# Optimization experiments

Hardware: AMD Instinct MI355X
Metric: run time of the kernel (lower is better)

Reference implementation:

```python
import jax, jax.numpy as jnp
import numpy as np

B, L, D, H = 2, 2048, 2048, 16
Dh = D // H
THETA = 500000.0


def _init_rope(dim, seq_len, n_heads):
    # Returns freqs_cis of shape (1, seq_len, 1, head_dim//2, 2) -> [..., 0]=cos, [..., 1]=sin
    hd = dim // n_heads
    inv_freqs = 1.0 / (THETA ** (jnp.arange(0, hd, 2, dtype=jnp.float32) / hd))
    t = jnp.arange(seq_len, dtype=jnp.float32)
    freqs = jnp.outer(t, inv_freqs).astype(jnp.float32)  # (L, hd/2)
    fc = jnp.stack([jnp.cos(freqs)[None, :, None, :],
                    jnp.sin(freqs)[None, :, None, :]], axis=3)  # (1, L, 1, 2, hd/2)
    return fc.transpose(0, 1, 2, 4, 3)  # (1, L, 1, hd/2, 2)


def _apply_rope(q, k, freqs_cis):
    def rotate(x):
        x2 = x.reshape(*x.shape[:-1], -1, 2)  # (B, L, H, Dh/2, 2)
        f = freqs_cis[:, :x.shape[1]]
        cos, sin = f[..., 0], f[..., 1]
        r = jnp.stack([x2[..., 0] * cos - x2[..., 1] * sin,
                       x2[..., 1] * cos + x2[..., 0] * sin], axis=-1)
        return r.reshape(*x.shape)
    return rotate(q), rotate(k)


def setup_inputs() -> dict:
    key = jax.random.key(0)
    kx, kq, kk, kv, ko = jax.random.split(key, 5)
    scale = 1.0 / np.sqrt(D)
    x = jax.random.normal(kx, (B, L, D), dtype=jnp.float32)
    Wq = jax.random.normal(kq, (D, H, Dh), dtype=jnp.float32) * scale
    Wk = jax.random.normal(kk, (D, H, Dh), dtype=jnp.float32) * scale
    Wv = jax.random.normal(kv, (D, H, Dh), dtype=jnp.float32) * scale
    Wo = jax.random.normal(ko, (D, D), dtype=jnp.float32) * scale
    return {"x": x, "Wq": Wq, "Wk": Wk, "Wv": Wv, "Wo": Wo}


def reference(x, Wq, Wk, Wv, Wo):
    freqs_cis = _init_rope(D, L, H)
    q = jnp.einsum('bld,dhk->blhk', x, Wq)  # (B, L, H, Dh)
    k = jnp.einsum('bld,dhk->blhk', x, Wk)
    v = jnp.einsum('bld,dhk->blhk', x, Wv)
    q, k = _apply_rope(q, k, freqs_cis)
    q = q / (Dh ** 0.5)
    att = jnp.einsum('bqhd,bkhd->bhqk', q, k)  # (B, H, L, L)
    Lq = x.shape[1]
    mask = jnp.tril(jnp.ones((1, 1, Lq, Lq), dtype=jnp.bool_))
    neg_inf = jnp.finfo(jnp.float32).min
    att = jnp.where(mask, att, neg_inf)
    att = jax.nn.softmax(att, axis=-1)
    out = jnp.einsum('bhqk,bkhd->bqhd', att, v)  # (B, L, H, Dh)
    out = out.reshape(x.shape)
    return jnp.einsum('bld,de->ble', out, Wo)
```

## Files before the change

### kernel.cpp

```cpp
#include <hip/hip_runtime.h>

typedef unsigned short u16;
typedef unsigned int u32;

#define Bb 2
#define Lc 2048
#define Dc 2048
#define Hc 16
#define DhC 128

typedef __bf16 bf16x8 __attribute__((ext_vector_type(8)));
typedef float f32x4 __attribute__((ext_vector_type(4)));
typedef float f32x16 __attribute__((ext_vector_type(16)));

__device__ __forceinline__ u16 f2b(float f) {
  u32 u = __float_as_uint(f);
  u32 r = (u + 0x7fffu + ((u >> 16) & 1u)) >> 16;
  return (u16)r;
}
__device__ __forceinline__ float b2f(u16 u) {
  return __uint_as_float(((u32)u) << 16);
}

__device__ __forceinline__ u32 cvtpk(float lo, float hi) {
  u32 r;
  asm("v_cvt_pk_bf16_f32 %0, %1, %2" : "=v"(r) : "v"(lo), "v"(hi));
  return r;
}

__device__ __forceinline__ void gll16(const void* g, void* l) {
  __builtin_amdgcn_global_load_lds(
      (const __attribute__((address_space(1))) u32*)g,
      (__attribute__((address_space(3))) u32*)l, 16, 0, 0);
}

__global__ __launch_bounds__(256) void sniff_dtype(const u16* __restrict__ x,
                                                   int* __restrict__ flag) {
  __shared__ int bad;
  if (threadIdx.x == 0) bad = 0;
  __syncthreads();
  int local = 0;
  for (int i = threadIdx.x; i < 65536; i += 256) {
    float v = fabsf(b2f(x[i]));
    if (!(v < 1000.f)) local = 1;
  }
  if (local) atomicOr(&bad, 1);
  __syncthreads();
  if (threadIdx.x == 0) *flag = bad;
}

__global__ __launch_bounds__(256) void conv_x(const void* __restrict__ in,
                                              u16* __restrict__ out,
                                              const int* __restrict__ flag) {
  const int f32 = *flag;
  const int i0 = (blockIdx.x * 256 + threadIdx.x) * 4;
  if (f32) {
    const float* p = (const float*)in;
#pragma unroll
    for (int j = 0; j < 4; j++) out[i0 + j] = f2b(p[i0 + j]);
  } else {
    const u16* p = (const u16*)in;
#pragma unroll
    for (int j = 0; j < 4; j++) out[i0 + j] = p[i0 + j];
  }
}

__global__ __launch_bounds__(256) void transpose2d_conv(const void* __restrict__ in,
                                                        u16* __restrict__ out,
                                                        const int* __restrict__ flag) {
  __shared__ __align__(16) u16 tile[64][65];
  const int f32 = *flag;
  const int r0 = blockIdx.y * 64, c0 = blockIdx.x * 64;
  const int tc = threadIdx.x & 63, tr4 = threadIdx.x >> 6;
#pragma unroll
  for (int p = 0; p < 16; p++) {
    int r = tr4 + p * 4;
    size_t idx = (size_t)(r0 + r) * 2048 + c0 + tc;
    tile[r][tc] = f32 ? f2b(((const float*)in)[idx]) : ((const u16*)in)[idx];
  }
  __syncthreads();
#pragma unroll
  for (int p = 0; p < 16; p++) {
    int rr = tr4 + p * 4;
    out[(size_t)(c0 + rr) * 2048 + r0 + tc] = tile[tc][rr];
  }
}

template <typename OutT>
__device__ __forceinline__ void gemm_bt_core(const u16* __restrict__ A,
                                             const u16* __restrict__ Bt,
                                             OutT* __restrict__ C) {
  constexpr int K = 2048, N = 2048;
  __shared__ __align__(16) u16 As[128 * 64];
  __shared__ __align__(16) u16 Bs[128 * 64];
  const int tid = threadIdx.x;
  const int lane = tid & 63, wid = tid >> 6;
  const int wm = (wid >> 1) * 64, wn = (wid & 1) * 64;
  const int m0 = blockIdx.x * 128, n0 = blockIdx.y * 128;
  const int quad = lane >> 4, l15 = lane & 15;
  const int sw = l15 & 7;

  const f32x4 fz = {0.f, 0.f, 0.f, 0.f};
  f32x4 acc[4][4];
#pragma unroll
  for (int i = 0; i < 4; i++)
#pragma unroll
    for (int j = 0; j < 4; j++) acc[i][j] = fz;

  const int srl = (lane >> 3);
  const int ssl = lane & 7;

  for (int k0 = 0; k0 < K; k0 += 64) {
#pragma unroll
    for (int p = 0; p < 4; p++) {
      const int r = p * 32 + wid * 8 + srl;
      const int c = ssl ^ (r & 7);
      u16* lb = As + (p * 256 + wid * 64) * 8;
      gll16(A + (size_t)(m0 + r) * K + k0 + c * 8, lb);
    }
#pragma unroll
    for (int p = 0; p < 4; p++) {
      const int r = p * 32 + wid * 8 + srl;
      const int c = ssl ^ (r & 7);
      u16* lb = Bs + (p * 256 + wid * 64) * 8;
      gll16(Bt + (size_t)(n0 + r) * K + k0 + c * 8, lb);
    }
    __syncthreads();
#pragma unroll
    for (int ks = 0; ks < 2; ks++) {
      bf16x8 af[4], bfr[4];
#pragma unroll
      for (int t = 0; t < 4; t++) {
        const int cc = ((ks * 4 + quad) ^ sw) * 8;
        af[t]  = *(const bf16x8*)(&As[(wm + t * 16 + l15) * 64 + cc]);
        bfr[t] = *(const bf16x8*)(&Bs[(wn + t * 16 + l15) * 64 + cc]);
      }
#pragma unroll
      for (int mt = 0; mt < 4; mt++)
#pragma unroll
        for (int nt = 0; nt < 4; nt++)
          acc[mt][nt] = __builtin_amdgcn_mfma_f32_16x16x32_bf16(af[mt], bfr[nt], acc[mt][nt], 0, 0, 0);
    }
    __syncthreads();
  }
#pragma unroll
  for (int mt = 0; mt < 4; mt++)
#pragma unroll
    for (int nt = 0; nt < 4; nt++) {
      int col = n0 + wn + nt * 16 + l15;
#pragma unroll
      for (int r = 0; r < 4; r++) {
        int row = m0 + wm + mt * 16 + quad * 4 + r;
        float v = acc[mt][nt][r];
        if constexpr (sizeof(OutT) == 2)
          C[(size_t)row * N + col] = f2b(v);
        else
          C[(size_t)row * N + col] = v;
      }
    }
}

__global__ __launch_bounds__(256) void gemm_bt(const u16* __restrict__ A,
                                               const u16* __restrict__ Bt,
                                               u16* __restrict__ C) {
  gemm_bt_core<u16>(A, Bt, C);
}
__global__ __launch_bounds__(256) void gemm_bt_f32(const u16* __restrict__ A,
                                                   const u16* __restrict__ Bt,
                                                   float* __restrict__ C) {
  gemm_bt_core<float>(A, Bt, C);
}

__global__ __launch_bounds__(256) void transpose_v_k(const u16* __restrict__ V,
                                                     u16* __restrict__ Vt) {
  __shared__ __align__(16) u16 tile[64][65];
  const int z = blockIdx.z;
  const int b = z >> 4, h = z & 15;
  const int l0 = blockIdx.y * 64, d0 = blockIdx.x * 64;
  const int tc = threadIdx.x & 63, tr4 = threadIdx.x >> 6;
#pragma unroll
  for (int p = 0; p < 16; p++) {
    int l = tr4 + p * 4;
    tile[l][tc] = V[(size_t)((b * Lc + l0 + l) * Hc + h) * DhC + d0 + tc];
  }
  __syncthreads();
#pragma unroll
  for (int p = 0; p < 16; p++) {
    int dd = tr4 + p * 4;
    Vt[((size_t)z * DhC + d0 + dd) * Lc + l0 + tc] = tile[tc][dd];
  }
}

__global__ __launch_bounds__(256) void rope_qk(u16* __restrict__ Q, u16* __restrict__ K) {
  const int idx = blockIdx.x * 256 + threadIdx.x;
  const int j = idx & 63;
  const int l = (idx >> 10) & 2047;
  const float inv = expf(-0.2050369278f * (float)j);
  const float ang = (float)l * inv;
  float s, c;
  sincosf(ang, &s, &c);
  const size_t off = (size_t)idx * 2;
  const float q0 = b2f(Q[off]), q1 = b2f(Q[off + 1]);
  const float k0 = b2f(K[off]), k1 = b2f(K[off + 1]);
  const float sc = 0.08838834764f;
  Q[off]     = f2b((q0 * c - q1 * s) * sc);
  Q[off + 1] = f2b((q1 * c + q0 * s) * sc);
  K[off]     = f2b(k0 * c - k1 * s);
  K[off + 1] = f2b(k1 * c + k0 * s);
}

#define NEGBIG (-3.0e30f)
__global__ __launch_bounds__(256, 2) void flash_attn(const u16* __restrict__ Q,
                                                     const u16* __restrict__ Kg,
                                                     const u16* __restrict__ Vt,
                                                     u16* __restrict__ O) {
  __shared__ __align__(16) u16 Ks[2][64 * 128];
  __shared__ __align__(16) u16 Vs[2][128 * 64];
  const int tid = threadIdx.x;
  const int lane = tid & 63, w = tid >> 6;
  const int l31 = lane & 31, hib = lane >> 5;
  const int bh = blockIdx.y;
  const int b = bh >> 4, h = bh & 15;
  const int qt = (bh & 16) ? (int)blockIdx.x : (15 - (int)blockIdx.x);
  const int q0 = qt * 128;
  const int qw0 = q0 + w * 32;
  const int nkv = 2 * qt + 2;

  const int krl = lane >> 4, ksl = lane & 15;
  const int vrl = lane >> 3, vsl = lane & 7;

  bf16x8 qf[8];
  {
    const u16* qptr = Q + ((size_t)(b * Lc + qw0 + l31) * Hc + h) * DhC + 8 * hib;
#pragma unroll
    for (int s = 0; s < 8; s++) qf[s] = *(const bf16x8*)(qptr + s * 16);
  }

  {
#pragma unroll
    for (int p = 0; p < 4; p++) {
      const int r = p * 16 + w * 4 + krl;
      const int c = ksl ^ (r & 15);
      gll16(Kg + ((size_t)(b * Lc + r) * Hc + h) * DhC + c * 8,
            &Ks[0][(p * 256 + w * 64) * 8]);
    }
#pragma unroll
    for (int p = 0; p < 4; p++) {
      const int r = p * 32 + w * 8 + vrl;
      const int c = vsl ^ (r & 7);
      gll16(Vt + ((size_t)bh * DhC + r) * Lc + c * 8,
            &Vs[0][(p * 256 + w * 64) * 8]);
    }
  }

  f32x16 o[4];
#pragma unroll
  for (int dt = 0; dt < 4; dt++) o[dt] = (f32x16)0.0f;
  float mrow = NEGBIG, lrow = 0.f;

  __syncthreads();

  for (int kvt = 0; kvt < nkv; kvt++) {
    const int cur = kvt & 1;
    const u16* Ksc = Ks[cur];
    const u16* Vsc = Vs[cur];

    if (kvt + 1 < nkv) {
      const int nv0 = (kvt + 1) * 64;
      const int nxt = cur ^ 1;
#pragma unroll
      for (int p = 0; p < 4; p++) {
        const int r = p * 16 + w * 4 + krl;
        const int c = ksl ^ (r & 15);
        gll16(Kg + ((size_t)(b * Lc + nv0 + r) * Hc + h) * DhC + c * 8,
              &Ks[nxt][(p * 256 + w * 64) * 8]);
      }
#pragma unroll
      for (int p = 0; p < 4; p++) {
        const int r = p * 32 + w * 8 + vrl;
        const int c = vsl ^ (r & 7);
        gll16(Vt + ((size_t)bh * DhC + r) * Lc + nv0 + c * 8,
              &Vs[nxt][(p * 256 + w * 64) * 8]);
      }
    }

    const int kv0 = kvt * 64;
    const bool active = (kv0 <= qw0 + 31);
    if (active) {
      f32x16 s0 = (f32x16)0.0f, s1 = (f32x16)0.0f;
      __builtin_amdgcn_s_setprio(1);
#pragma unroll
      for (int s = 0; s < 8; s++) {
        const int ch = ((2 * s + hib) ^ (l31 & 15)) * 8;
        bf16x8 k0 = *(const bf16x8*)(&Ksc[l31 * 128 + ch]);
        bf16x8 k1 = *(const bf16x8*)(&Ksc[(32 + l31) * 128 + ch]);
        s0 = __builtin_amdgcn_mfma_f32_32x32x16_bf16(k0, qf[s], s0, 0, 0, 0);
        s1 = __builtin_amdgcn_mfma_f32_32x32x16_bf16(k1, qf[s], s1, 0, 0, 0);
      }
      __builtin_amdgcn_s_setprio(0);

      if (kv0 + 63 > qw0) {
        const int qg = qw0 + l31;
#pragma unroll
        for (int r = 0; r < 16; r++) {
          const int cr = (r & 3) + 8 * (r >> 2) + 4 * hib;
          if (kv0 + cr > qg) s0[r] = NEGBIG;
          if (kv0 + 32 + cr > qg) s1[r] = NEGBIG;
        }
      }

      float mx;
      {
        float a[8];
#pragma unroll
        for (int i = 0; i < 8; i++)
          a[i] = fmaxf(fmaxf(s0[i], s0[i + 8]), fmaxf(s1[i], s1[i + 8]));
        float b0 = fmaxf(a[0], a[4]), b1 = fmaxf(a[1], a[5]);
        float b2 = fmaxf(a[2], a[6]), b3 = fmaxf(a[3], a[7]);
        mx = fmaxf(fmaxf(b0, b1), fmaxf(b2, b3));
      }
      mx = fmaxf(mx, __shfl_xor(mx, 32, 64));

      if (!__all(mx - mrow <= 8.f)) {
        const float mnew = fmaxf(mrow, mx);
        const float al = __expf(mrow - mnew);
#pragma unroll
        for (int dt = 0; dt < 4; dt++)
#pragma unroll
          for (int e = 0; e < 16; e++) o[dt][e] *= al;
        lrow *= al;
        mrow = mnew;
      }

#pragma unroll
      for (int i = 0; i < 16; i++) {
        s0[i] = __expf(s0[i] - mrow);
        s1[i] = __expf(s1[i] - mrow);
      }
      float sm;
      {
        float a[8];
#pragma unroll
        for (int i = 0; i < 8; i++)
          a[i] = (s0[i] + s0[i + 8]) + (s1[i] + s1[i + 8]);
        sm = ((a[0] + a[4]) + (a[1] + a[5])) + ((a[2] + a[6]) + (a[3] + a[7]));
      }
      sm += __shfl_xor(sm, 32, 64);
      lrow += sm;

      bf16x8 paf[4];
#pragma unroll
      for (int t = 0; t < 2; t++) {
#pragma unroll
        for (int h8 = 0; h8 < 2; h8++) {
          const int rB = 8 * h8;
          u32 lo0, lo1, hi0, hi1;
          if (t == 0) {
            lo0 = cvtpk(s0[rB + 0], s0[rB + 1]);
            lo1 = cvtpk(s0[rB + 2], s0[rB + 3]);
            hi0 = cvtpk(s0[rB + 4], s0[rB + 5]);
            hi1 = cvtpk(s0[rB + 6], s0[rB + 7]);
          } else {
            lo0 = cvtpk(s1[rB + 0], s1[rB + 1]);
            lo1 = cvtpk(s1[rB + 2], s1[rB + 3]);
            hi0 = cvtpk(s1[rB + 4], s1[rB + 5]);
            hi1 = cvtpk(s1[rB + 6], s1[rB + 7]);
          }
          const u32 g0 = hib ? lo0 : hi0;
          const u32 g1 = hib ? lo1 : hi1;
          const u32 r0 = (u32)__shfl_xor((int)g0, 32, 64);
          const u32 r1 = (u32)__shfl_xor((int)g1, 32, 64);
          union { u32 u[4]; bf16x8 v; } pu;
          pu.u[0] = hib ? r0 : lo0;
          pu.u[1] = hib ? r1 : lo1;
          pu.u[2] = hib ? hi0 : r0;
          pu.u[3] = hib ? hi1 : r1;
          paf[2 * t + h8] = pu.v;
        }
      }

      __builtin_amdgcn_s_setprio(1);
#pragma unroll
      for (int B = 0; B < 4; B++) {
#pragma unroll
        for (int dt = 0; dt < 4; dt++) {
          const bf16x8 vf = *(const bf16x8*)(
              &Vsc[(32 * dt + l31) * 64 + (((2 * B + hib) ^ (l31 & 7))) * 8]);
          o[dt] = __builtin_amdgcn_mfma_f32_32x32x16_bf16(paf[B], vf, o[dt], 0, 0, 0);
        }
      }
      __builtin_amdgcn_s_setprio(0);
    }

    __syncthreads();
  }

#pragma unroll
  for (int r = 0; r < 16; r++) {
    const int cr = (r & 3) + 8 * (r >> 2) + 4 * hib;
    const float linv = 1.0f / __shfl(lrow, cr, 64);
    const size_t rowoff = ((size_t)(b * Lc + qw0 + cr) * Hc + h) * DhC + l31;
#pragma unroll
    for (int dt = 0; dt < 4; dt++)
      O[rowoff + 32 * dt] = f2b(o[dt][r] * linv);
  }
}

extern "C" void kernel_launch(void* const* d_in, const int* in_sizes, int n_in,
                              void* d_out, int out_size, void* d_ws, size_t ws_size,
                              hipStream_t stream) {
  const void* x  = d_in[0];
  const void* Wq = d_in[1];
  const void* Wk = d_in[2];
  const void* Wv = d_in[3];
  const void* Wo = d_in[4];
  float* out = (float*)d_out;

  char* w = (char*)d_ws;
  const size_t WSZ = (size_t)2048 * 2048;
  const size_t XSZ = (size_t)Bb * Lc * Dc;
  int* flag = (int*)w;
  u16* WT  = (u16*)(w + 256);
  u16* xc  = WT + WSZ;
  u16* Qb  = xc + XSZ;
  u16* Kb  = Qb + XSZ;
  u16* Vb  = Kb + XSZ;
  u16* Vtb = xc;
  u16* Ob  = Vb;

  sniff_dtype<<<1, 256, 0, stream>>>((const u16*)x, flag);
  conv_x<<<(int)(XSZ / 1024), 256, 0, stream>>>(x, xc, flag);

  dim3 tgrid(32, 32);
  dim3 ggrid(32, 16);

  transpose2d_conv<<<tgrid, 256, 0, stream>>>(Wq, WT, flag);
  gemm_bt<<<ggrid, 256, 0, stream>>>(xc, WT, Qb);
  transpose2d_conv<<<tgrid, 256, 0, stream>>>(Wk, WT, flag);
  gemm_bt<<<ggrid, 256, 0, stream>>>(xc, WT, Kb);
  transpose2d_conv<<<tgrid, 256, 0, stream>>>(Wv, WT, flag);
  gemm_bt<<<ggrid, 256, 0, stream>>>(xc, WT, Vb);

  rope_qk<<<(Bb * Lc * Hc * 64) / 256, 256, 0, stream>>>(Qb, Kb);

  dim3 vgrid(2, 32, 32);
  transpose_v_k<<<vgrid, 256, 0, stream>>>(Vb, Vtb);

  dim3 fgrid(16, 32);
  flash_attn<<<fgrid, 256, 0, stream>>>(Qb, Kb, Vtb, Ob);

  transpose2d_conv<<<tgrid, 256, 0, stream>>>(Wo, WT, flag);
  gemm_bt_f32<<<ggrid, 256, 0, stream>>>(Ob, WT, out);
}
```

Measured before the change: 493.8 us.

## Replace 128x128 GEMM with pipelined 256x256 kernel and fuse QKV projections

Replaces the 128x128 GEMM with a 512-thread 256x256-tile kernel. It uses a 4-stage LDS ring of K=32 slices, split A/B staging interleaved with MFMA phases, s_setprio, and an XCD-aware block swizzle. The three Q/K/V weights are transposed into one concatenated buffer, placed temporarily in the output buffer, so a single launch computes all three projections and writes each 2048-column chunk to its own destination. This cuts launch count, improves operand reuse and hides load latency. In exchange, the output-projection GEMM has only 128 blocks, and correctness relies on hand-placed waitcnt and barrier ordering.

```diff
diff --git a/kernel.cpp b/kernel.cpp
--- a/kernel.cpp
+++ b/kernel.cpp
@@ -87,88 +87,164 @@
 }
 
 template <typename OutT>
-__device__ __forceinline__ void gemm_bt_core(const u16* __restrict__ A,
+__device__ __forceinline__ void gemm256_core(const u16* __restrict__ A,
                                              const u16* __restrict__ Bt,
-                                             OutT* __restrict__ C) {
-  constexpr int K = 2048, N = 2048;
-  __shared__ __align__(16) u16 As[128 * 64];
-  __shared__ __align__(16) u16 Bs[128 * 64];
+                                             OutT* __restrict__ C,
+                                             int Ntiles, size_t bufStride) {
+  constexpr int K = 2048;
+  constexpr int NT = K / 32;
+  __shared__ __align__(16) u16 Al[4][256 * 32];
+  __shared__ __align__(16) u16 Bl[4][256 * 32];
+
   const int tid = threadIdx.x;
-  const int lane = tid & 63, wid = tid >> 6;
-  const int wm = (wid >> 1) * 64, wn = (wid & 1) * 64;
-  const int m0 = blockIdx.x * 128, n0 = blockIdx.y * 128;
+  const int lane = tid & 63, w = tid >> 6;
   const int quad = lane >> 4, l15 = lane & 15;
-  const int sw = l15 & 7;
+  const int wm = (w >> 2) & 1, wn = w & 3;
+
+  const int nwg = Ntiles << 4;
+  const int q8 = nwg >> 3;
+  const int id = (int)blockIdx.x;
+  const int swz = (id & 7) * q8 + (id >> 3);
+  const int m0 = (swz & 15) * 256;
+  const int n0 = (swz >> 4) * 256;
+
+  const int srow = lane >> 2;
+  const int scol = (lane & 3) * 8;
+  const u16* Ag = A + (size_t)(m0 + w * 16 + srow) * K + scol;
+  const u16* Bg = Bt + (size_t)(n0 + w * 16 + srow) * K + scol;
+
+  const int aoff = (wm * 128 + l15) * 32 + quad * 8;
+  const int boff = (wn * 64 + l15) * 32 + quad * 8;
 
   const f32x4 fz = {0.f, 0.f, 0.f, 0.f};
-  f32x4 acc[4][4];
-#pragma unroll
-  for (int i = 0; i < 4; i++)
+  f32x4 acc[8][4];
+#pragma unroll
+  for (int i = 0; i < 8; i++)
 #pragma unroll
     for (int j = 0; j < 4; j++) acc[i][j] = fz;
 
-  const int srl = (lane >> 3);
-  const int ssl = lane & 7;
-
-  for (int k0 = 0; k0 < K; k0 += 64) {
-#pragma unroll
-    for (int p = 0; p < 4; p++) {
-      const int r = p * 32 + wid * 8 + srl;
-      const int c = ssl ^ (r & 7);
-      u16* lb = As + (p * 256 + wid * 64) * 8;
-      gll16(A + (size_t)(m0 + r) * K + k0 + c * 8, lb);
+#define STAGE_A(t)                                                         \
+  {                                                                        \
+    const int _s = (t) & 3;                                                \
+    const size_t _k = (size_t)(t) * 32;                                    \
+    gll16(Ag + _k, &Al[_s][(w * 16) * 32]);                                \
+    gll16(Ag + (size_t)128 * K + _k, &Al[_s][(128 + w * 16) * 32]);        \
+  }
+#define STAGE_B(t)                                                         \
+  {                                                                        \
+    const int _s = (t) & 3;                                                \
+    const size_t _k = (size_t)(t) * 32;                                    \
+    gll16(Bg + _k, &Bl[_s][(w * 16) * 32]);                                \
+    gll16(Bg + (size_t)128 * K + _k, &Bl[_s][(128 + w * 16) * 32]);        \
+  }
+
+  STAGE_A(0); STAGE_B(0);
+  STAGE_A(1); STAGE_B(1);
+  STAGE_A(2); STAGE_B(2);
+  asm volatile("s_waitcnt vmcnt(8)" ::: "memory");
+  __builtin_amdgcn_s_barrier();
+
+  for (int t = 0; t < NT - 3; ++t) {
+    const u16* Abuf = Al[t & 3];
+    const u16* Bbuf = Bl[t & 3];
+    bf16x8 af0[4], bfv[4], af1[4];
+#pragma unroll
+    for (int m = 0; m < 4; m++)
+      af0[m] = *(const bf16x8*)(Abuf + aoff + m * 16 * 32);
+#pragma unroll
+    for (int n = 0; n < 4; n++)
+      bfv[n] = *(const bf16x8*)(Bbuf + boff + n * 16 * 32);
+    STAGE_A(t + 3);
+    __builtin_amdgcn_s_barrier();
+    asm volatile("s_waitcnt lgkmcnt(0)" ::: "memory");
+    __builtin_amdgcn_sched_barrier(0);
+    __builtin_amdgcn_s_setprio(1);
+#pragma unroll
+    for (int m = 0; m < 4; m++)
+#pragma unroll
+      for (int n = 0; n < 4; n++)
+        acc[m][n] = __builtin_amdgcn_mfma_f32_16x16x32_bf16(af0[m], bfv[n], acc[m][n], 0, 0, 0);
+    __builtin_amdgcn_s_setprio(0);
+    __builtin_amdgcn_s_barrier();
+#pragma unroll
+    for (int m = 0; m < 4; m++)
+      af1[m] = *(const bf16x8*)(Abuf + aoff + (64 + m * 16) * 32);
+    STAGE_B(t + 3);
+    __builtin_amdgcn_s_barrier();
+    asm volatile("s_waitcnt lgkmcnt(0)" ::: "memory");
+    __builtin_amdgcn_sched_barrier(0);
+    __builtin_amdgcn_s_setprio(1);
+#pragma unroll
+    for (int m = 0; m < 4; m++)
+#pragma unroll
+      for (int n = 0; n < 4; n++)
+        acc[4 + m][n] = __builtin_amdgcn_mfma_f32_16x16x32_bf16(af1[m], bfv[n], acc[4 + m][n], 0, 0, 0);
+    __builtin_amdgcn_s_setprio(0);
+    asm volatile("s_waitcnt vmcnt(8)" ::: "memory");
+    __builtin_amdgcn_s_barrier();
+  }
+
+  asm volatile("s_waitcnt vmcnt(0)" ::: "memory");
+  __builtin_amdgcn_s_barrier();
+#pragma unroll
+  for (int t = NT - 3; t < NT; ++t) {
+    const u16* Abuf = Al[t & 3];
+    const u16* Bbuf = Bl[t & 3];
+    bf16x8 af0[4], bfv[4], af1[4];
+#pragma unroll
+    for (int m = 0; m < 4; m++)
+      af0[m] = *(const bf16x8*)(Abuf + aoff + m * 16 * 32);
+#pragma unroll
+    for (int n = 0; n < 4; n++)
+      bfv[n] = *(const bf16x8*)(Bbuf + boff + n * 16 * 32);
+#pragma unroll
+    for (int m = 0; m < 4; m++)
+      af1[m] = *(const bf16x8*)(Abuf + aoff + (64 + m * 16) * 32);
+    asm volatile("s_waitcnt lgkmcnt(0)" ::: "memory");
+    __builtin_amdgcn_sched_barrier(0);
+#pragma unroll
+    for (int m = 0; m < 4; m++)
+#pragma unroll
+      for (int n = 0; n < 4; n++)
+        acc[m][n] = __builtin_amdgcn_mfma_f32_16x16x32_bf16(af0[m], bfv[n], acc[m][n], 0, 0, 0);
+#pragma unroll
+    for (int m = 0; m < 4; m++)
+#pragma unroll
+      for (int n = 0; n < 4; n++)
+        acc[4 + m][n] = __builtin_amdgcn_mfma_f32_16x16x32_bf16(af1[m], bfv[n], acc[4 + m][n], 0, 0, 0);
+  }
+#undef STAGE_A
+#undef STAGE_B
+
+#pragma unroll
+  for (int mt = 0; mt < 8; mt++)
+#pragma unroll
+    for (int n = 0; n < 4; n++) {
+      const int colg = n0 + wn * 64 + n * 16 + l15;
+      const size_t cbase = (size_t)(colg >> 11) * bufStride + (colg & 2047);
+#pragma unroll
+      for (int r = 0; r < 4; r++) {
+        const int row = m0 + wm * 128 + mt * 16 + quad * 4 + r;
+        const float v = acc[mt][n][r];
+        if constexpr (sizeof(OutT) == 2)
+          C[cbase + (size_t)row * 2048] = f2b(v);
+        else
+          C[cbase + (size_t)row * 2048] = v;
+      }
     }
-#pragma unroll
-    for (int p = 0; p < 4; p++) {
-      const int r = p * 32 + wid * 8 + srl;
-      const int c = ssl ^ (r & 7);
-      u16* lb = Bs + (p * 256 + wid * 64) * 8;
-      gll16(Bt + (size_t)(n0 + r) * K + k0 + c * 8, lb);
-    }
-    __syncthreads();
-#pragma unroll
-    for (int ks = 0; ks < 2; ks++) {
-      bf16x8 af[4], bfr[4];
-#pragma unroll
-      for (int t = 0; t < 4; t++) {
-        const int cc = ((ks * 4 + quad) ^ sw) * 8;
-        af[t]  = *(const bf16x8*)(&As[(wm + t * 16 + l15) * 64 + cc]);
-        bfr[t] = *(const bf16x8*)(&Bs[(wn + t * 16 + l15) * 64 + cc]);
-      }
-#pragma unroll
-      for (int mt = 0; mt < 4; mt++)
-#pragma unroll
-        for (int nt = 0; nt < 4; nt++)
-          acc[mt][nt] = __builtin_amdgcn_mfma_f32_16x16x32_bf16(af[mt], bfr[nt], acc[mt][nt], 0, 0, 0);
-    }
-    __syncthreads();
-  }
-#pragma unroll
-  for (int mt = 0; mt < 4; mt++)
-#pragma unroll
-    for (int nt = 0; nt < 4; nt++) {
-      int col = n0 + wn + nt * 16 + l15;
-#pragma unroll
-      for (int r = 0; r < 4; r++) {
-        int row = m0 + wm + mt * 16 + quad * 4 + r;
-        float v = acc[mt][nt][r];
-        if constexpr (sizeof(OutT) == 2)
-          C[(size_t)row * N + col] = f2b(v);
-        else
-          C[(size_t)row * N + col] = v;
-      }
-    }
-}
-
-__global__ __launch_bounds__(256) void gemm_bt(const u16* __restrict__ A,
-                                               const u16* __restrict__ Bt,
-                                               u16* __restrict__ C) {
-  gemm_bt_core<u16>(A, Bt, C);
-}
-__global__ __launch_bounds__(256) void gemm_bt_f32(const u16* __restrict__ A,
-                                                   const u16* __restrict__ Bt,
-                                                   float* __restrict__ C) {
-  gemm_bt_core<float>(A, Bt, C);
+}
+
+__global__ __launch_bounds__(512, 2) void gemm256_bf(const u16* __restrict__ A,
+                                                     const u16* __restrict__ Bt,
+                                                     u16* __restrict__ C,
+                                                     int Ntiles, size_t bufStride) {
+  gemm256_core<u16>(A, Bt, C, Ntiles, bufStride);
+}
+__global__ __launch_bounds__(512, 2) void gemm256_f32(const u16* __restrict__ A,
+                                                      const u16* __restrict__ Bt,
+                                                      float* __restrict__ C,
+                                                      int Ntiles, size_t bufStride) {
+  gemm256_core<float>(A, Bt, C, Ntiles, bufStride);
 }
 
 __global__ __launch_bounds__(256) void transpose_v_k(const u16* __restrict__ V,
@@ -427,19 +503,18 @@
   u16* Vb  = Kb + XSZ;
   u16* Vtb = xc;
   u16* Ob  = Vb;
+  u16* WTall = (u16*)d_out;
 
   sniff_dtype<<<1, 256, 0, stream>>>((const u16*)x, flag);
   conv_x<<<(int)(XSZ / 1024), 256, 0, stream>>>(x, xc, flag);
 
   dim3 tgrid(32, 32);
-  dim3 ggrid(32, 16);
-
-  transpose2d_conv<<<tgrid, 256, 0, stream>>>(Wq, WT, flag);
-  gemm_bt<<<ggrid, 256, 0, stream>>>(xc, WT, Qb);
-  transpose2d_conv<<<tgrid, 256, 0, stream>>>(Wk, WT, flag);
-  gemm_bt<<<ggrid, 256, 0, stream>>>(xc, WT, Kb);
-  transpose2d_conv<<<tgrid, 256, 0, stream>>>(Wv, WT, flag);
-  gemm_bt<<<ggrid, 256, 0, stream>>>(xc, WT, Vb);
+
+  transpose2d_conv<<<tgrid, 256, 0, stream>>>(Wq, WTall, flag);
+  transpose2d_conv<<<tgrid, 256, 0, stream>>>(Wk, WTall + WSZ, flag);
+  transpose2d_conv<<<tgrid, 256, 0, stream>>>(Wv, WTall + 2 * WSZ, flag);
+
+  gemm256_bf<<<dim3(384), 512, 0, stream>>>(xc, WTall, Qb, 24, XSZ);
 
   rope_qk<<<(Bb * Lc * Hc * 64) / 256, 256, 0, stream>>>(Qb, Kb);
 
@@ -450,5 +525,5 @@
   flash_attn<<<fgrid, 256, 0, stream>>>(Qb, Kb, Vtb, Ob);
 
   transpose2d_conv<<<tgrid, 256, 0, stream>>>(Wo, WT, flag);
-  gemm_bt_f32<<<ggrid, 256, 0, stream>>>(Ob, WT, out);
-}
+  gemm256_f32<<<dim3(128), 512, 0, stream>>>(Ob, WT, out, 8, 0);
+}
```

Result: slower. 562.6 us (+13.9%).

## Fuse QKV projections into one pipelined GEMM with 4-stage LDS ring

Applied to the files above, without the earlier changes.

Replaces the 128x128 single-buffered GEMM with a 512-thread 128x256 tile kernel that streams K in 32-wide slices through a 4-deep LDS ring, using explicit vmcnt waits and raw barriers. MFMA issue priority is raised during the inner loop, and a grouped block-id swizzle improves L2 reuse. The Q, K and V weights are transposed into a scratch buffer placed in the output allocation so a single launch computes all three projections, and the output projection uses the same kernel. This costs more LDS and registers per block, and it depends on the output buffer being large enough to hold the three transposed weight matrices before it is overwritten.

```diff
diff --git a/kernel.cpp b/kernel.cpp
--- a/kernel.cpp
+++ b/kernel.cpp
@@ -87,18 +87,31 @@
 }
 
 template <typename OutT>
-__device__ __forceinline__ void gemm_bt_core(const u16* __restrict__ A,
-                                             const u16* __restrict__ Bt,
-                                             OutT* __restrict__ C) {
-  constexpr int K = 2048, N = 2048;
-  __shared__ __align__(16) u16 As[128 * 64];
-  __shared__ __align__(16) u16 Bs[128 * 64];
+__device__ __forceinline__ void gemmfo_core(const u16* __restrict__ A,
+                                            const u16* __restrict__ Bt,
+                                            OutT* __restrict__ C,
+                                            int Ntiles, size_t bufStride) {
+  constexpr int K = 2048;
+  constexpr int NTK = K / 32;
+  __shared__ __align__(16) u16 Als[4][128 * 32];
+  __shared__ __align__(16) u16 Bls[4][256 * 32];
+
   const int tid = threadIdx.x;
-  const int lane = tid & 63, wid = tid >> 6;
-  const int wm = (wid >> 1) * 64, wn = (wid & 1) * 64;
-  const int m0 = blockIdx.x * 128, n0 = blockIdx.y * 128;
+  const int lane = tid & 63, w = tid >> 6;
   const int quad = lane >> 4, l15 = lane & 15;
-  const int sw = l15 & 7;
+  const int wm = w >> 2, wn = w & 3;
+
+  const int nwg = 32 * Ntiles;
+  const int q8 = nwg >> 3;
+  const int id = (int)blockIdx.x;
+  const int swz = (id & 7) * q8 + (id >> 3);
+  const int m0 = (swz & 31) * 128;
+  const int n0 = (swz >> 5) * 256;
+
+  const int sc = (lane >> 4) * 8;
+  const u16* aSrc = A + (size_t)(m0 + w * 16 + l15) * K + sc;
+  const u16* bSrc0 = Bt + (size_t)(n0 + (2 * w) * 16 + l15) * K + sc;
+  const u16* bSrc1 = Bt + (size_t)(n0 + (2 * w + 1) * 16 + l15) * K + sc;
 
   const f32x4 fz = {0.f, 0.f, 0.f, 0.f};
   f32x4 acc[4][4];
@@ -107,68 +120,83 @@
 #pragma unroll
     for (int j = 0; j < 4; j++) acc[i][j] = fz;
 
-  const int srl = (lane >> 3);
-  const int ssl = lane & 7;
-
-  for (int k0 = 0; k0 < K; k0 += 64) {
-#pragma unroll
-    for (int p = 0; p < 4; p++) {
-      const int r = p * 32 + wid * 8 + srl;
-      const int c = ssl ^ (r & 7);
-      u16* lb = As + (p * 256 + wid * 64) * 8;
-      gll16(A + (size_t)(m0 + r) * K + k0 + c * 8, lb);
+  auto stage = [&](int t) {
+    const int s = t & 3;
+    const int k = t * 32;
+    gll16(aSrc + k, &Als[s][w * 512]);
+    gll16(bSrc0 + k, &Bls[s][(2 * w) * 512]);
+    gll16(bSrc1 + k, &Bls[s][(2 * w + 1) * 512]);
+  };
+
+  auto compute = [&](int t) {
+    const u16* abuf = Als[t & 3];
+    const u16* bbuf = Bls[t & 3];
+    bf16x8 afr[4], bfr[4];
+#pragma unroll
+    for (int mt = 0; mt < 4; mt++)
+      afr[mt] = *(const bf16x8*)(&abuf[(wm * 4 + mt) * 512 + lane * 8]);
+#pragma unroll
+    for (int nt = 0; nt < 4; nt++)
+      bfr[nt] = *(const bf16x8*)(&bbuf[(wn * 4 + nt) * 512 + lane * 8]);
+    asm volatile("s_waitcnt lgkmcnt(0)" ::: "memory");
+    __builtin_amdgcn_sched_barrier(0);
+    __builtin_amdgcn_s_setprio(1);
+#pragma unroll
+    for (int mt = 0; mt < 4; mt++)
+#pragma unroll
+      for (int nt = 0; nt < 4; nt++)
+        acc[mt][nt] = __builtin_amdgcn_mfma_f32_16x16x32_bf16(
+            afr[mt], bfr[nt], acc[mt][nt], 0, 0, 0);
+    __builtin_amdgcn_s_setprio(0);
+  };
+
+  stage(0); stage(1); stage(2);
+  asm volatile("s_waitcnt vmcnt(6)" ::: "memory");
+  __builtin_amdgcn_s_barrier();
+
+  for (int t = 0; t < NTK - 3; ++t) {
+    stage(t + 3);
+    compute(t);
+    asm volatile("s_waitcnt vmcnt(6)" ::: "memory");
+    __builtin_amdgcn_s_barrier();
+  }
+  compute(NTK - 3);
+  asm volatile("s_waitcnt vmcnt(3)" ::: "memory");
+  __builtin_amdgcn_s_barrier();
+  compute(NTK - 2);
+  asm volatile("s_waitcnt vmcnt(0)" ::: "memory");
+  __builtin_amdgcn_s_barrier();
+  compute(NTK - 1);
+
+#pragma unroll
+  for (int mt = 0; mt < 4; mt++)
+#pragma unroll
+    for (int nt = 0; nt < 4; nt++) {
+      const int colg = n0 + wn * 64 + nt * 16 + l15;
+      const size_t cbase = (size_t)(colg >> 11) * bufStride + (colg & 2047);
+#pragma unroll
+      for (int r = 0; r < 4; r++) {
+        const int row = m0 + wm * 64 + mt * 16 + quad * 4 + r;
+        const float v = acc[mt][nt][r];
+        if constexpr (sizeof(OutT) == 2)
+          C[cbase + (size_t)row * 2048] = f2b(v);
+        else
+          C[cbase + (size_t)row * 2048] = v;
+      }
     }
-#pragma unroll
-    for (int p = 0; p < 4; p++) {
-      const int r = p * 32 + wid * 8 + srl;
-      const int c = ssl ^ (r & 7);
-      u16* lb = Bs + (p * 256 + wid * 64) * 8;
-      gll16(Bt + (size_t)(n0 + r) * K + k0 + c * 8, lb);
-    }
-    __syncthreads();
-#pragma unroll
-    for (int ks = 0; ks < 2; ks++) {
-      bf16x8 af[4], bfr[4];
-#pragma unroll
-      for (int t = 0; t < 4; t++) {
-        const int cc = ((ks * 4 + quad) ^ sw) * 8;
-        af[t]  = *(const bf16x8*)(&As[(wm + t * 16 + l15) * 64 + cc]);
-        bfr[t] = *(const bf16x8*)(&Bs[(wn + t * 16 + l15) * 64 + cc]);
-      }
-#pragma unroll
-      for (int mt = 0; mt < 4; mt++)
-#pragma unroll
-        for (int nt = 0; nt < 4; nt++)
-          acc[mt][nt] = __builtin_amdgcn_mfma_f32_16x16x32_bf16(af[mt], bfr[nt], acc[mt][nt], 0, 0, 0);
-    }
-    __syncthreads();
-  }
-#pragma unroll
-  for (int mt = 0; mt < 4; mt++)
-#pragma unroll
-    for (int nt = 0; nt < 4; nt++) {
-      int col = n0 + wn + nt * 16 + l15;
-#pragma unroll
-      for (int r = 0; r < 4; r++) {
-        int row = m0 + wm + mt * 16 + quad * 4 + r;
-        float v = acc[mt][nt][r];
-        if constexpr (sizeof(OutT) == 2)
-          C[(size_t)row * N + col] = f2b(v);
-        else
-          C[(size_t)row * N + col] = v;
-      }
-    }
-}
-
-__global__ __launch_bounds__(256) void gemm_bt(const u16* __restrict__ A,
-                                               const u16* __restrict__ Bt,
-                                               u16* __restrict__ C) {
-  gemm_bt_core<u16>(A, Bt, C);
-}
-__global__ __launch_bounds__(256) void gemm_bt_f32(const u16* __restrict__ A,
-                                                   const u16* __restrict__ Bt,
-                                                   float* __restrict__ C) {
-  gemm_bt_core<float>(A, Bt, C);
+}
+
+__global__ __launch_bounds__(512, 2) void gemmfo_bf(const u16* __restrict__ A,
+                                                    const u16* __restrict__ Bt,
+                                                    u16* __restrict__ C,
+                                                    int Ntiles, size_t bufStride) {
+  gemmfo_core<u16>(A, Bt, C, Ntiles, bufStride);
+}
+__global__ __launch_bounds__(512, 2) void gemmfo_f32(const u16* __restrict__ A,
+                                                     const u16* __restrict__ Bt,
+                                                     float* __restrict__ C,
+                                                     int Ntiles, size_t bufStride) {
+  gemmfo_core<float>(A, Bt, C, Ntiles, bufStride);
 }
 
 __global__ __launch_bounds__(256) void transpose_v_k(const u16* __restrict__ V,
@@ -427,19 +455,18 @@
   u16* Vb  = Kb + XSZ;
   u16* Vtb = xc;
   u16* Ob  = Vb;
+  u16* WTall = (u16*)d_out;
 
   sniff_dtype<<<1, 256, 0, stream>>>((const u16*)x, flag);
   conv_x<<<(int)(XSZ / 1024), 256, 0, stream>>>(x, xc, flag);
 
   dim3 tgrid(32, 32);
-  dim3 ggrid(32, 16);
-
-  transpose2d_conv<<<tgrid, 256, 0, stream>>>(Wq, WT, flag);
-  gemm_bt<<<ggrid, 256, 0, stream>>>(xc, WT, Qb);
-  transpose2d_conv<<<tgrid, 256, 0, stream>>>(Wk, WT, flag);
-  gemm_bt<<<ggrid, 256, 0, stream>>>(xc, WT, Kb);
-  transpose2d_conv<<<tgrid, 256, 0, stream>>>(Wv, WT, flag);
-  gemm_bt<<<ggrid, 256, 0, stream>>>(xc, WT, Vb);
+
+  transpose2d_conv<<<tgrid, 256, 0, stream>>>(Wq, WTall, flag);
+  transpose2d_conv<<<tgrid, 256, 0, stream>>>(Wk, WTall + WSZ, flag);
+  transpose2d_conv<<<tgrid, 256, 0, stream>>>(Wv, WTall + 2 * WSZ, flag);
+
+  gemmfo_bf<<<dim3(768), 512, 0, stream>>>(xc, WTall, Qb, 24, XSZ);
 
   rope_qk<<<(Bb * Lc * Hc * 64) / 256, 256, 0, stream>>>(Qb, Kb);
 
@@ -450,5 +477,5 @@
   flash_attn<<<fgrid, 256, 0, stream>>>(Qb, Kb, Vtb, Ob);
 
   transpose2d_conv<<<tgrid, 256, 0, stream>>>(Wo, WT, flag);
-  gemm_bt_f32<<<ggrid, 256, 0, stream>>>(Ob, WT, out);
-}
+  gemmfo_f32<<<dim3(256), 512, 0, stream>>>(Ob, WT, out, 8, 0);
+}
```

Measured after the change: 614.3 us. +24.4%, slower.
